# Optimization experiments

Hardware: AMD Instinct MI355X
Metric: run time of the kernel (lower is better)

## Reference

```python
import jax, jax.numpy as jnp
import numpy as np

CA, CZ, CS, CSI = 128, 128, 384, 256
NH, HD, NB, A = 8, 16, 6, 7
RMAX, SMAX = 32, 2
RELP_DIM = 4 * (RMAX + 1) + 1 + 2 * (SMAX + 1)  # 139


def make_relp(L):
    # single-chain relative-position features: [L, L, 139]
    i = jnp.arange(L)
    d = i[:, None] - i[None, :]
    a_rel_pos = jax.nn.one_hot(jnp.clip(d + RMAX, 0, 2 * RMAX), 2 * (RMAX + 1))
    d_tok = jnp.where(d == 0, RMAX, 2 * RMAX + 1)  # same-res only on diagonal
    a_rel_tok = jax.nn.one_hot(d_tok, 2 * (RMAX + 1))
    same_ent = jnp.ones((L, L, 1), jnp.float32)
    a_rel_chain = jax.nn.one_hot(jnp.full((L, L), SMAX), 2 * (SMAX + 1))
    return jnp.concatenate([a_rel_pos, a_rel_tok, same_ent, a_rel_chain], axis=-1)


def ln(x, g, b):
    m = x.mean(-1, keepdims=True)
    v = ((x - m) ** 2).mean(-1, keepdims=True)
    return (x - m) / jnp.sqrt(v + 1e-5) * g + b


def setup_inputs():
    key = jax.random.key(0)
    ks = iter(jax.random.split(key, 64))
    def p(*shape):
        return (jax.random.normal(next(ks), shape, jnp.float32) * 0.05)
    B, Ns, L = 1, 2, 384
    inp = dict(
        x_t=jax.random.normal(next(ks), (B, Ns, L, A, 3), jnp.float32),
        sigma=jax.random.uniform(next(ks), (B, Ns), jnp.float32),
        s_inputs=jax.random.normal(next(ks), (B, L, CSI), jnp.float32),
        s_trunk=jax.random.normal(next(ks), (B, L, CS), jnp.float32),
        z_trunk=jax.random.normal(next(ks), (B, L, L, CZ), jnp.float32),
        token_mask=jnp.ones((B, L), bool),
        s_in_w=p(CSI, CS), s_in_b=p(CS),
        relp_w=p(RELP_DIM, CZ), relp_b=p(CZ),
        t1_w=p(1, CS), t1_b=p(CS), t2_w=p(CS, CS), t2_b=p(CS),
        xp_w=p(3 * A, CA), xp_b=p(CA),
        s2a_w=p(CS, CA), s2a_b=p(CA),
        out_w=p(CA, 3 * A), out_b=p(3 * A),
        an_g=jnp.ones((NB, CA)), an_b=jnp.zeros((NB, CA)),
        zn_g=jnp.ones((NB, CZ)), zn_b=jnp.zeros((NB, CZ)),
        qw=p(NB, CA, CA), qb=p(NB, CA),
        kw=p(NB, CA, CA), kb=p(NB, CA),
        vw=p(NB, CA, CA), vb=p(NB, CA),
        zw=p(NB, CZ, NH), zb=p(NB, NH),
        ow=p(NB, CA, CA), ob=p(NB, CA),
        f1w=p(NB, CA, 4 * CA), f1b=p(NB, 4 * CA),
        f2w=p(NB, 4 * CA, CA), f2b=p(NB, CA),
    )
    return inp


def reference(x_t, sigma, s_inputs, s_trunk, z_trunk, token_mask,
              s_in_w, s_in_b, relp_w, relp_b, t1_w, t1_b, t2_w, t2_b,
              xp_w, xp_b, s2a_w, s2a_b, out_w, out_b,
              an_g, an_b, zn_g, zn_b, qw, qb, kw, kb, vw, vb,
              zw, zb, ow, ob, f1w, f1b, f2w, f2b):
    B, Ns, L = x_t.shape[:3]
    relp = make_relp(L)                                   # [L, L, 139]
    pair_z = z_trunk + relp @ relp_w + relp_b             # [B, L, L, CZ]
    s_cond = s_trunk + s_inputs @ s_in_w + s_in_b         # [B, L, CS]
    t_feat = jax.nn.silu(sigma.reshape(B * Ns, 1) @ t1_w + t1_b) @ t2_w + t2_b
    single_s = s_cond[:, None] + t_feat.reshape(B, Ns, CS)[:, :, None]  # [B,Ns,L,CS]
    a = x_t.reshape(B, Ns, L, 3 * A) @ xp_w + xp_b + single_s @ s2a_w + s2a_b
    a2 = a.reshape(B * Ns, L, CA)
    z2 = jnp.broadcast_to(pair_z[:, None], (B, Ns, L, L, CZ)).reshape(B * Ns, L, L, CZ)
    m = jnp.broadcast_to(token_mask[:, None], (B, Ns, L)).reshape(B * Ns, L)
    pair_mask = m[:, :, None] & m[:, None, :]             # [B*Ns, L, L]
    scale = 1.0 / np.sqrt(HD).astype(np.float32)
    for i in range(NB):
        an = ln(a2, an_g[i], an_b[i])
        zn = ln(z2, zn_g[i], zn_b[i])
        q = (an @ qw[i] + qb[i]).reshape(-1, L, NH, HD)
        k = (an @ kw[i] + kb[i]).reshape(-1, L, NH, HD)
        v = (an @ vw[i] + vb[i]).reshape(-1, L, NH, HD)
        logits = jnp.einsum('blhd,bmhd->bhlm', q, k) * scale
        bias = (zn @ zw[i] + zb[i]).transpose(0, 3, 1, 2)  # [B*Ns, NH, L, L]
        logits = jnp.where(pair_mask[:, None], logits + bias, -1e9)
        attn = jax.nn.softmax(logits, axis=-1)
        o = jnp.einsum('bhlm,bmhd->blhd', attn, v).reshape(-1, L, CA)
        a2 = a2 + (o @ ow[i] + ob[i])
        an2 = ln(a2, an_g[i], an_b[i])
        a2 = a2 + jax.nn.gelu(an2 @ f1w[i] + f1b[i], approximate=False) @ f2w[i] + f2b[i]
    vout = (a2 @ out_w + out_b).reshape(B, Ns, L, A, 3)
    return vout * token_mask[:, None, :, None, None].astype(vout.dtype)
```

## Files before the change

### kernel.cpp

```cpp
#include <hip/hip_runtime.h>
#include <math.h>

#define L 384
#define CA 128
#define NH 8
#define HD 16
#define NB 6
#define NS 2
#define NP (L*L)

typedef __attribute__((ext_vector_type(4))) float f32x4;
typedef __attribute__((ext_vector_type(8))) short s16x8;
typedef __attribute__((ext_vector_type(4))) unsigned short u16x4;
typedef unsigned short ushort_t;

__device__ inline unsigned short f2bf(float f){
  union { float f; unsigned int u; } v; v.f = f;
  unsigned int u = v.u;
  unsigned int r = u + 0x7FFF + ((u>>16)&1);
  return (unsigned short)(r>>16);
}
__device__ inline float bf2f(ushort_t u){
  union { float f; unsigned int i; } v; v.i = ((unsigned int)u)<<16; return v.f;
}

#define WT_LAYER 196608
__global__ __launch_bounds__(256) void k_prep(
    const float* qw, const float* kw, const float* vw,
    const float* f1w, const float* f2w, const float* ow,
    const float* relp_w, const float* relp_b,
    const float* s_in_w, const float* s2a_w,
    const float* sigma, const float* t1w, const float* t1b,
    const float* t2w, const float* t2b,
    const float* zng, const float* znb, const float* zw, const float* zb,
    ushort_t* wT, ushort_t* wzT, float* rbase, float* cb, float* t_feat,
    ushort_t* s_in_wT, ushort_t* s2a_wT){
  int b = blockIdx.x, t = threadIdx.x;
  if(b == 324){
    for(int idx=t; idx<6144; idx+=256){
      int h = idx>>7, c = idx&127;
      wzT[h*128+c] = f2bf(zng[(h>>3)*128+c]*zw[((h>>3)*128+c)*8+(h&7)]);
    }
    if(t<128) rbase[t] = relp_w[132*128+t] + relp_w[135*128+t] + relp_b[t];
    if(t<48){
      int blk=t>>3, hh=t&7;
      float acc = zb[t];
      for(int c=0;c<128;c++) acc += znb[blk*128+c]*zw[(blk*128+c)*8+hh];
      cb[t] = acc;
    }
    return;
  }
  if(b == 325){
    __shared__ float sil[2][384];
    for(int i=t;i<768;i+=256){
      int s=i/384, k=i%384;
      float x = sigma[s]*t1w[k] + t1b[k];
      sil[s][k] = x / (1.f + expf(-x));
    }
    __syncthreads();
    for(int o=t;o<768;o+=256){
      int s=o/384, c=o%384;
      float acc = t2b[c];
      for(int k=0;k<384;k++) acc += sil[s][k]*t2w[k*384+c];
      t_feat[s*384+c] = acc;
    }
    return;
  }
  __shared__ float tl[64][65];
  const float* src; ushort_t* dst;
  int M, N, k0, n0;
  if(b < 96){
    int mat = b>>2, li = mat>>2, wsel = mat&3, tile = b&3;
    const float* const ws_[4] = {qw, kw, vw, ow};
    const int off_[4] = {0, 16384, 32768, 180224};
    src = ws_[wsel] + (size_t)li*16384;
    dst = wT + (size_t)li*WT_LAYER + off_[wsel];
    M = 128; N = 128; k0 = (tile>>1)*64; n0 = (tile&1)*64;
  } else if(b < 192){
    int idx = b-96, li = idx>>4, tile = idx&15;
    src = f1w + (size_t)li*65536;
    dst = wT + (size_t)li*WT_LAYER + 49152;
    M = 128; N = 512; k0 = (tile>>3)*64; n0 = (tile&7)*64;
  } else if(b < 288){
    int idx = b-192, li = idx>>4, tile = idx&15;
    src = f2w + (size_t)li*65536;
    dst = wT + (size_t)li*WT_LAYER + 114688;
    M = 512; N = 128; k0 = (tile>>1)*64; n0 = (tile&1)*64;
  } else if(b < 312){
    int tile = b-288;
    src = s_in_w; dst = s_in_wT;
    M = 256; N = 384; k0 = (tile/6)*64; n0 = (tile%6)*64;
  } else {
    int tile = b-312;
    src = s2a_w; dst = s2a_wT;
    M = 384; N = 128; k0 = (tile>>1)*64; n0 = (tile&1)*64;
  }
  for(int i=t;i<4096;i+=256){
    int r=i>>6, c=i&63;
    tl[r][c] = src[(size_t)(k0+r)*N + n0+c];
  }
  __syncthreads();
  for(int i=t;i<4096;i+=256){
    int r=i>>6, c=i&63;
    dst[(size_t)(n0+r)*M + k0+c] = f2bf(tl[c][r]);
  }
}

__global__ __launch_bounds__(256) void k2_bias(
    const float* z_trunk, const float* relp_w, const float* rbase,
    const ushort_t* wzT, const float* cb, ushort_t* bias_all){
  __shared__ float lds_c[48][65];
  int t = threadIdx.x, lane = t&63, wv = t>>6;
  int rowf = lane&15, kg = lane>>4;
  int p = blockIdx.x*64 + wv*16 + rowf;
  int i = p/L, j = p - i*L, d = i - j;
  int r1 = d+32; r1 = r1<0?0:(r1>64?64:r1);
  int r2 = (d==0) ? 98 : 131;
  const float* zp  = z_trunk + (size_t)p*128;
  const float* w1p = relp_w + r1*128;
  const float* w2p = relp_w + r2*128;

  float val[4][8];
  float s = 0.f;
  #pragma unroll
  for(int ks=0; ks<4; ks++){
    int c0 = ks*32 + kg*8;
    f32x4 za = *(const f32x4*)(zp +c0), zb2 = *(const f32x4*)(zp +c0+4);
    f32x4 wa = *(const f32x4*)(w1p+c0), wb = *(const f32x4*)(w1p+c0+4);
    f32x4 ua = *(const f32x4*)(w2p+c0), ub = *(const f32x4*)(w2p+c0+4);
    f32x4 ra = *(const f32x4*)(rbase+c0), rb = *(const f32x4*)(rbase+c0+4);
    #pragma unroll
    for(int jj=0;jj<4;jj++){
      val[ks][jj]   = za[jj]+wa[jj]+ua[jj]+ra[jj];
      val[ks][jj+4] = zb2[jj]+wb[jj]+ub[jj]+rb[jj];
      s += val[ks][jj] + val[ks][jj+4];
    }
  }
  s += __shfl_xor(s,16,64); s += __shfl_xor(s,32,64);
  float mean = s*(1.f/128.f);
  float q2 = 0.f;
  #pragma unroll
  for(int ks=0; ks<4; ks++)
    #pragma unroll
    for(int jj=0;jj<8;jj++){ float dd = val[ks][jj]-mean; q2 += dd*dd; }
  q2 += __shfl_xor(q2,16,64); q2 += __shfl_xor(q2,32,64);
  float rstd = rsqrtf(q2*(1.f/128.f) + 1e-5f);

  s16x8 af[4];
  #pragma unroll
  for(int ks=0; ks<4; ks++)
    #pragma unroll
    for(int jj=0;jj<8;jj++) af[ks][jj] = (short)f2bf((val[ks][jj]-mean)*rstd);

  #pragma unroll
  for(int ht=0; ht<3; ht++){
    int col = ht*16 + rowf;
    float cbv = cb[col];
    f32x4 acc = {cbv,cbv,cbv,cbv};
    #pragma unroll
    for(int ks=0; ks<4; ks++){
      s16x8 bf = *(const s16x8*)&wzT[col*128 + ks*32 + kg*8];
      acc = __builtin_amdgcn_mfma_f32_16x16x32_bf16(af[ks], bf, acc, 0,0,0);
    }
    #pragma unroll
    for(int i2=0;i2<4;i2++) lds_c[col][wv*16 + kg*4 + i2] = acc[i2];
  }
  __syncthreads();
  int p0 = blockIdx.x*64;
  int i0 = p0/L, qt_ = i0>>4, q16 = i0&15, j0 = p0 - i0*L;
  for(int idx=t; idx<3072; idx+=256){
    int pl = idx>>6, c = idx&63;
    int li_ = pl>>3, h_ = pl&7;
    bias_all[(size_t)((li_*24+qt_)*8+h_)*6144 + q16*384 + j0 + c] = f2bf(lds_c[pl][c]);
  }
}

__device__ inline void qkv_project(ushort_t zh[16][152], const ushort_t* wTl,
                                   const float* qb, const float* kb, const float* vb,
                                   ushort_t* q_bf, ushort_t* k_bf, ushort_t* vT_bf,
                                   int s_idx, int lbase, int wv, int rowf, int kg){
  s16x8 af[4];
  #pragma unroll
  for(int ks=0;ks<4;ks++) af[ks] = *(const s16x8*)&zh[rowf][ks*32 + kg*8];
  #pragma unroll
  for(int u=0;u<6;u++){
    int unit = wv*6 + u;
    int proj = unit>>3, nt = unit&7;
    int col = nt*16 + rowf;
    const ushort_t* wp = wTl + proj*16384;
    const float* bias = proj==0? qb : (proj==1? kb : vb);
    float bv = bias[col];
    f32x4 acc = {bv,bv,bv,bv};
    #pragma unroll
    for(int ks=0;ks<4;ks++){
      s16x8 bf = *(const s16x8*)&wp[col*128 + ks*32 + kg*8];
      acc = __builtin_amdgcn_mfma_f32_16x16x32_bf16(af[ks], bf, acc, 0,0,0);
    }
    int sh = s_idx*NH + nt;
    if(proj==2){
      #pragma unroll
      for(int i2=0;i2<4;i2++)
        vT_bf[((size_t)sh*16 + rowf)*384 + lbase + kg*4 + i2] = f2bf(acc[i2]);
    } else {
      float sc = (proj==0)? 0.25f : 1.0f;
      ushort_t* outp = (proj==0)? q_bf : k_bf;
      #pragma unroll
      for(int i2=0;i2<4;i2++)
        outp[((size_t)sh*384 + lbase + kg*4 + i2)*16 + rowf] = f2bf(acc[i2]*sc);
    }
  }
}

__global__ __launch_bounds__(256) void k_qkv0(
    const float* x_t, const float* s_inputs, const float* s_trunk,
    const float* s_in_b, const ushort_t* s_in_wT,
    const float* s2a_b, const ushort_t* s2a_wT,
    const float* xp_w, const float* xp_b, const float* t_feat,
    const float* g, const float* bb,
    const ushort_t* wTl, const float* qb, const float* kb, const float* vb,
    float* a2, ushort_t* q_bf, ushort_t* k_bf, ushort_t* vT_bf){
  __shared__ ushort_t si[16][280];
  __shared__ ushort_t scb[16][408];
  __shared__ float xrow[16][21];
  __shared__ float a_new[16][132];
  __shared__ ushort_t zh[16][152];
  int t = threadIdx.x, lane = t&63, wv = t>>6;
  int rowf = lane&15, kg = lane>>4;
  int bid = blockIdx.x, s_idx = bid/24, lt = bid%24;
  int lr0 = lt*16;

  for(int i=t;i<16*256;i+=256){
    int r=i>>8, c=i&255;
    si[r][c] = f2bf(s_inputs[(size_t)(lr0+r)*256+c]);
  }
  for(int i=t;i<16*21;i+=256){
    int r=i/21, u=i%21;
    xrow[r][u] = x_t[((size_t)s_idx*L + lr0 + r)*21 + u];
  }
  __syncthreads();

  {
    s16x8 af1[8];
    #pragma unroll
    for(int ks=0;ks<8;ks++) af1[ks] = *(const s16x8*)&si[rowf][ks*32+kg*8];
    const float* tf = t_feat + s_idx*384;
    #pragma unroll
    for(int nn=0;nn<6;nn++){
      int col = (wv*6+nn)*16 + rowf;
      float bv = s_in_b[col];
      f32x4 acc = {bv,bv,bv,bv};
      #pragma unroll
      for(int ks=0;ks<8;ks++){
        s16x8 bf = *(const s16x8*)&s_in_wT[col*256 + ks*32 + kg*8];
        acc = __builtin_amdgcn_mfma_f32_16x16x32_bf16(af1[ks], bf, acc, 0,0,0);
      }
      float tfc = tf[col];
      #pragma unroll
      for(int i2=0;i2<4;i2++){
        int r = kg*4+i2;
        scb[r][col] = f2bf(acc[i2] + s_trunk[(size_t)(lr0+r)*384+col] + tfc);
      }
    }
  }
  __syncthreads();

  {
    s16x8 xf[12];
    #pragma unroll
    for(int ks=0;ks<12;ks++) xf[ks] = *(const s16x8*)&scb[rowf][ks*32+kg*8];
    #pragma unroll
    for(int nn=0;nn<2;nn++){
      int col = (wv*2+nn)*16 + rowf;
      float base = xp_b[col] + s2a_b[col];
      f32x4 acc;
      #pragma unroll
      for(int i2=0;i2<4;i2++){
        float xc = base;
        #pragma unroll
        for(int u=0;u<21;u++) xc += xrow[kg*4+i2][u]*xp_w[u*128+col];
        acc[i2] = xc;
      }
      #pragma unroll
      for(int ks=0;ks<12;ks++){
        s16x8 bf = *(const s16x8*)&s2a_wT[col*384 + ks*32 + kg*8];
        acc = __builtin_amdgcn_mfma_f32_16x16x32_bf16(xf[ks], bf, acc, 0,0,0);
      }
      #pragma unroll
      for(int i2=0;i2<4;i2++){
        int r = kg*4+i2;
        a_new[r][col] = acc[i2];
        a2[((size_t)(s_idx*L + lr0 + r))*128 + col] = acc[i2];
      }
    }
  }
  __syncthreads();

  {
    int row = t>>4, sub = t&15;
    const float* xp = &a_new[row][sub*8];
    f32x4 x0 = *(const f32x4*)xp;
    f32x4 x1 = *(const f32x4*)(xp+4);
    float s = x0[0]+x0[1]+x0[2]+x0[3]+x1[0]+x1[1]+x1[2]+x1[3];
    s += __shfl_xor(s,1,64); s += __shfl_xor(s,2,64);
    s += __shfl_xor(s,4,64); s += __shfl_xor(s,8,64);
    float mean = s*(1.f/128.f);
    float q2 = 0.f;
    #pragma unroll
    for(int jj=0;jj<4;jj++){ float d0=x0[jj]-mean, d1=x1[jj]-mean; q2 += d0*d0+d1*d1; }
    q2 += __shfl_xor(q2,1,64); q2 += __shfl_xor(q2,2,64);
    q2 += __shfl_xor(q2,4,64); q2 += __shfl_xor(q2,8,64);
    float rstd = rsqrtf(q2*(1.f/128.f)+1e-5f);
    int c0 = sub*8;
    f32x4 g0 = *(const f32x4*)(g+c0), g1 = *(const f32x4*)(g+c0+4);
    f32x4 b0 = *(const f32x4*)(bb+c0), b1 = *(const f32x4*)(bb+c0+4);
    s16x8 pack;
    #pragma unroll
    for(int jj=0;jj<4;jj++){
      pack[jj]   = (short)f2bf((x0[jj]-mean)*rstd*g0[jj]+b0[jj]);
      pack[jj+4] = (short)f2bf((x1[jj]-mean)*rstd*g1[jj]+b1[jj]);
    }
    *(s16x8*)&zh[row][c0] = pack;
  }
  __syncthreads();
  qkv_project(zh, wTl, qb, kb, vb, q_bf, k_bf, vT_bf, s_idx, lr0, wv, rowf, kg);
}

__global__ __launch_bounds__(1024) void k_fused(
    float* a2, const float* an_g, const float* an_b, const ushort_t* wT,
    const float* qb_all, const float* kb_all, const float* vb_all,
    const float* ob_all, const float* f1b_all, const float* f2b_all,
    ushort_t* q_bf, ushort_t* k_bf, ushort_t* vT_bf,
    const ushort_t* bias_all, const float* out_w, const float* out_b,
    float* out, int li){
  __shared__ float orow[16][132];
  __shared__ float ocomb[8][16][20];
  __shared__ float lcomb[8][16];
  union SM {
    struct {
      ushort_t bias[8][16][392];
      ushort_t P[16][16][72];
    } fl;
    struct {
      float a_new[16][132];
      ushort_t zh[16][152];
      ushort_t h_lds[16][536];
      float fcomb[8][16][20];
    } post;
  };
  __shared__ SM sm;

  int t = threadIdx.x, lane = t&63, wv = t>>6;
  int rowf = lane&15, kg = lane>>4;
  int bid = blockIdx.x, s_idx = bid/24, qt = bid%24;
  int r0 = bid*16;
  const ushort_t* wTl = wT + (size_t)li*WT_LAYER;
  const float* g  = an_g + li*128;
  const float* bb = an_b + li*128;

  {
    const ushort_t* btile = bias_all + (size_t)(li*24+qt)*8*6144;
    #pragma unroll
    for(int it=0; it<6; it++){
      int idx = t + it*1024;
      int row2 = idx/48, seg = idx%48;
      *(s16x8*)&sm.fl.bias[row2>>4][row2&15][seg*8] =
          *(const s16x8*)&btile[(size_t)row2*384 + seg*8];
    }
  }
  __syncthreads();

  {
    int h = wv>>1, kh = wv&1;
    int sh = s_idx*NH + h;
    ushort_t (*Pw)[72] = sm.fl.P[wv];
    s16x8 qf = {0,0,0,0,0,0,0,0};
    if(kg < 2) qf = *(const s16x8*)&q_bf[((size_t)sh*384 + qt*16 + rowf)*16 + kg*8];
    const ushort_t* kp = k_bf + (size_t)sh*384*16;
    const ushort_t* vp = vT_bf + ((size_t)sh*16 + rowf)*384;

    f32x4 o0 = {0,0,0,0}, o1 = {0,0,0,0};
    float l_acc = 0.f;
    for(int c=0;c<3;c++){
      int key0 = kh*192 + c*64;
      f32x4 st[4];
      #pragma unroll
      for(int t4=0;t4<4;t4++){
        s16x8 kf = {0,0,0,0,0,0,0,0};
        if(kg < 2) kf = *(const s16x8*)&kp[((size_t)(key0 + t4*16 + rowf))*16 + kg*8];
        u16x4 bb4 = *(const u16x4*)&sm.fl.bias[h][rowf][key0 + t4*16 + kg*4];
        f32x4 cin;
        #pragma unroll
        for(int jj=0;jj<4;jj++) cin[jj] = bf2f(bb4[jj]);
        st[t4] = __builtin_amdgcn_mfma_f32_16x16x32_bf16(kf, qf, cin, 0,0,0);
      }
      #pragma unroll
      for(int t4=0;t4<4;t4++){
        float p0 = __expf(st[t4][0]), p1 = __expf(st[t4][1]);
        float p2 = __expf(st[t4][2]), p3 = __expf(st[t4][3]);
        l_acc += (p0+p1)+(p2+p3);
        u16x4 pk = {f2bf(p0), f2bf(p1), f2bf(p2), f2bf(p3)};
        *(u16x4*)&Pw[rowf][t4*16 + kg*4] = pk;
      }
      {
        s16x8 pa = *(const s16x8*)&Pw[rowf][kg*8];
        s16x8 vbf = *(const s16x8*)&vp[key0 + kg*8];
        o0 = __builtin_amdgcn_mfma_f32_16x16x32_bf16(pa, vbf, o0, 0,0,0);
        s16x8 pb = *(const s16x8*)&Pw[rowf][32 + kg*8];
        s16x8 vbf2 = *(const s16x8*)&vp[key0 + 32 + kg*8];
        o1 = __builtin_amdgcn_mfma_f32_16x16x32_bf16(pb, vbf2, o1, 0,0,0);
      }
    }
    f32x4 o_acc = o0 + o1;
    l_acc += __shfl_xor(l_acc, 16, 64);
    l_acc += __shfl_xor(l_acc, 32, 64);
    if(kh==1){
      #pragma unroll
      for(int i2=0;i2<4;i2++) ocomb[h][kg*4+i2][rowf] = o_acc[i2];
      if(kg==0) lcomb[h][rowf] = l_acc;
    }
    __syncthreads();
    if(kh==0){
      l_acc += lcomb[h][rowf];
      #pragma unroll
      for(int i2=0;i2<4;i2++) o_acc[i2] += ocomb[h][kg*4+i2][rowf];
      float inv = 1.f / l_acc;
      #pragma unroll
      for(int i2=0;i2<4;i2++){
        float invq = __shfl(inv, kg*4 + i2, 64);
        orow[kg*4+i2][h*16 + rowf] = o_acc[i2]*invq;
      }
    }
  }
  __syncthreads();

  if(wv < 8){
    s16x8 af[4];
    #pragma unroll
    for(int ks=0;ks<4;ks++){
      f32x4 v0 = *(const f32x4*)&orow[rowf][ks*32+kg*8];
      f32x4 v1 = *(const f32x4*)&orow[rowf][ks*32+kg*8+4];
      s16x8 p;
      #pragma unroll
      for(int jj=0;jj<4;jj++){ p[jj] = (short)f2bf(v0[jj]); p[jj+4] = (short)f2bf(v1[jj]); }
      af[ks] = p;
    }
    const ushort_t* wo = wTl + 180224;
    const float* obp = ob_all + li*128;
    int col = wv*16 + rowf;
    float bv = obp[col];
    f32x4 acc = {bv,bv,bv,bv};
    f32x4 accB = {0,0,0,0};
    #pragma unroll
    for(int ks=0;ks<2;ks++){
      s16x8 bf = *(const s16x8*)&wo[col*128 + ks*32 + kg*8];
      acc = __builtin_amdgcn_mfma_f32_16x16x32_bf16(af[ks], bf, acc, 0,0,0);
      s16x8 bf2 = *(const s16x8*)&wo[col*128 + (ks+2)*32 + kg*8];
      accB = __builtin_amdgcn_mfma_f32_16x16x32_bf16(af[ks+2], bf2, accB, 0,0,0);
    }
    acc += accB;
    #pragma unroll
    for(int i2=0;i2<4;i2++){
      int r = kg*4+i2;
      sm.post.a_new[r][col] = a2[(size_t)(r0+r)*128 + col] + acc[i2];
    }
  }
  __syncthreads();

  {
    int row = wv, c0 = lane*2;
    float x0 = sm.post.a_new[row][c0], x1 = sm.post.a_new[row][c0+1];
    float s = x0+x1;
    s += __shfl_xor(s,1,64); s += __shfl_xor(s,2,64); s += __shfl_xor(s,4,64);
    s += __shfl_xor(s,8,64); s += __shfl_xor(s,16,64); s += __shfl_xor(s,32,64);
    float mean = s*(1.f/128.f);
    float d0=x0-mean, d1=x1-mean;
    float q2 = d0*d0+d1*d1;
    q2 += __shfl_xor(q2,1,64); q2 += __shfl_xor(q2,2,64); q2 += __shfl_xor(q2,4,64);
    q2 += __shfl_xor(q2,8,64); q2 += __shfl_xor(q2,16,64); q2 += __shfl_xor(q2,32,64);
    float rstd = rsqrtf(q2*(1.f/128.f)+1e-5f);
    unsigned int pk = (unsigned int)f2bf(d0*rstd*g[c0]+bb[c0])
                    | ((unsigned int)f2bf(d1*rstd*g[c0+1]+bb[c0+1])<<16);
    *(unsigned int*)&sm.post.zh[row][c0] = pk;
  }
  __syncthreads();

  {
    s16x8 xf[4];
    #pragma unroll
    for(int ks=0;ks<4;ks++) xf[ks] = *(const s16x8*)&sm.post.zh[rowf][ks*32 + kg*8];
    const ushort_t* w1 = wTl + 49152;
    const float* f1bp = f1b_all + li*512;
    #pragma unroll
    for(int nn=0; nn<2; nn++){
      int col = (wv*2+nn)*16 + rowf;
      float bv = f1bp[col];
      f32x4 acc = {bv,bv,bv,bv};
      #pragma unroll
      for(int ks=0;ks<4;ks++){
        s16x8 bf = *(const s16x8*)&w1[col*128 + ks*32 + kg*8];
        acc = __builtin_amdgcn_mfma_f32_16x16x32_bf16(xf[ks], bf, acc, 0,0,0);
      }
      #pragma unroll
      for(int i2=0;i2<4;i2++){
        float x = acc[i2];
        float ge = 0.5f*x*(1.f + erff(x*0.70710678f));
        sm.post.h_lds[kg*4+i2][col] = f2bf(ge);
      }
    }
  }
  __syncthreads();

  {
    const ushort_t* w2 = wTl + 114688;
    const float* f2bp = f2b_all + li*128;
    int ct = wv>>1, kh2 = wv&1;
    int col2 = ct*16 + rowf;
    float bv = kh2? 0.f : f2bp[col2];
    f32x4 accA = {bv,bv,bv,bv};
    f32x4 accB = {0,0,0,0};
    int ks0 = kh2*8;
    #pragma unroll
    for(int kk=0; kk<4; kk++){
      s16x8 hfA = *(const s16x8*)&sm.post.h_lds[rowf][(ks0+kk)*32 + kg*8];
      s16x8 bfA = *(const s16x8*)&w2[col2*512 + (ks0+kk)*32 + kg*8];
      accA = __builtin_amdgcn_mfma_f32_16x16x32_bf16(hfA, bfA, accA, 0,0,0);
      s16x8 hfB = *(const s16x8*)&sm.post.h_lds[rowf][(ks0+kk+4)*32 + kg*8];
      s16x8 bfB = *(const s16x8*)&w2[col2*512 + (ks0+kk+4)*32 + kg*8];
      accB = __builtin_amdgcn_mfma_f32_16x16x32_bf16(hfB, bfB, accB, 0,0,0);
    }
    accA += accB;
    if(kh2==1){
      #pragma unroll
      for(int i2=0;i2<4;i2++) sm.post.fcomb[ct][kg*4+i2][rowf] = accA[i2];
    }
    __syncthreads();
    if(kh2==0){
      #pragma unroll
      for(int i2=0;i2<4;i2++){
        int r = kg*4+i2;
        float fin = sm.post.a_new[r][col2] + accA[i2] + sm.post.fcomb[ct][r][rowf];
        a2[(size_t)(r0+r)*128 + col2] = fin;
        sm.post.a_new[r][col2] = fin;
      }
    }
  }
  __syncthreads();

  if(li < NB-1){
    const float* g2  = an_g + (li+1)*128;
    const float* bb2 = an_b + (li+1)*128;
    {
      int row = wv, c0 = lane*2;
      float x0 = sm.post.a_new[row][c0], x1 = sm.post.a_new[row][c0+1];
      float s = x0+x1;
      s += __shfl_xor(s,1,64); s += __shfl_xor(s,2,64); s += __shfl_xor(s,4,64);
      s += __shfl_xor(s,8,64); s += __shfl_xor(s,16,64); s += __shfl_xor(s,32,64);
      float mean = s*(1.f/128.f);
      float d0=x0-mean, d1=x1-mean;
      float q2 = d0*d0+d1*d1;
      q2 += __shfl_xor(q2,1,64); q2 += __shfl_xor(q2,2,64); q2 += __shfl_xor(q2,4,64);
      q2 += __shfl_xor(q2,8,64); q2 += __shfl_xor(q2,16,64); q2 += __shfl_xor(q2,32,64);
      float rstd = rsqrtf(q2*(1.f/128.f)+1e-5f);
      unsigned int pk = (unsigned int)f2bf(d0*rstd*g2[c0]+bb2[c0])
                      | ((unsigned int)f2bf(d1*rstd*g2[c0+1]+bb2[c0+1])<<16);
      *(unsigned int*)&sm.post.zh[row][c0] = pk;
    }
    __syncthreads();
    {
      const ushort_t* wTn = wT + (size_t)(li+1)*WT_LAYER;
      const float* qb2 = qb_all + (li+1)*128;
      const float* kb2 = kb_all + (li+1)*128;
      const float* vb2 = vb_all + (li+1)*128;
      s16x8 af[4];
      #pragma unroll
      for(int ks=0;ks<4;ks++) af[ks] = *(const s16x8*)&sm.post.zh[rowf][ks*32 + kg*8];
      #pragma unroll
      for(int u=0;u<2;u++){
        int unit = wv + u*16;
        if(unit < 24){
          int proj = unit>>3, nt = unit&7;
          int col = nt*16 + rowf;
          const ushort_t* wp = wTn + proj*16384;
          const float* bias = proj==0? qb2 : (proj==1? kb2 : vb2);
          float bv = bias[col];
          f32x4 acc = {bv,bv,bv,bv};
          #pragma unroll
          for(int ks=0;ks<4;ks++){
            s16x8 bf = *(const s16x8*)&wp[col*128 + ks*32 + kg*8];
            acc = __builtin_amdgcn_mfma_f32_16x16x32_bf16(af[ks], bf, acc, 0,0,0);
          }
          int sh = s_idx*NH + nt;
          if(proj==2){
            #pragma unroll
            for(int i2=0;i2<4;i2++)
              vT_bf[((size_t)sh*16 + rowf)*384 + qt*16 + kg*4 + i2] = f2bf(acc[i2]);
          } else {
            float sc = (proj==0)? 0.25f : 1.0f;
            ushort_t* outp = (proj==0)? q_bf : k_bf;
            #pragma unroll
            for(int i2=0;i2<4;i2++)
              outp[((size_t)sh*384 + qt*16 + kg*4 + i2)*16 + rowf] = f2bf(acc[i2]*sc);
          }
        }
      }
    }
  } else {
    for(int idx=t; idx<336; idx+=1024){
      int r = idx/21, c = idx%21;
      float acc = out_b[c];
      #pragma unroll 8
      for(int kk=0;kk<128;kk++) acc += sm.post.a_new[r][kk]*out_w[kk*21+c];
      out[(size_t)(r0+r)*21 + c] = acc;
    }
  }
}

extern "C" void kernel_launch(void* const* d_in, const int* in_sizes, int n_in,
                              void* d_out, int out_size, void* d_ws, size_t ws_size,
                              hipStream_t stream){
  const float* x_t      = (const float*)d_in[0];
  const float* sigma    = (const float*)d_in[1];
  const float* s_inputs = (const float*)d_in[2];
  const float* s_trunk  = (const float*)d_in[3];
  const float* z_trunk  = (const float*)d_in[4];
  const float* s_in_w = (const float*)d_in[6];
  const float* s_in_b = (const float*)d_in[7];
  const float* relp_w = (const float*)d_in[8];
  const float* relp_b = (const float*)d_in[9];
  const float* t1_w = (const float*)d_in[10];
  const float* t1_b = (const float*)d_in[11];
  const float* t2_w = (const float*)d_in[12];
  const float* t2_b = (const float*)d_in[13];
  const float* xp_w = (const float*)d_in[14];
  const float* xp_b = (const float*)d_in[15];
  const float* s2a_w = (const float*)d_in[16];
  const float* s2a_b = (const float*)d_in[17];
  const float* out_w = (const float*)d_in[18];
  const float* out_b = (const float*)d_in[19];
  const float* an_g = (const float*)d_in[20];
  const float* an_b = (const float*)d_in[21];
  const float* zn_g = (const float*)d_in[22];
  const float* zn_b = (const float*)d_in[23];
  const float* qw = (const float*)d_in[24];
  const float* qb = (const float*)d_in[25];
  const float* kw = (const float*)d_in[26];
  const float* kb = (const float*)d_in[27];
  const float* vw = (const float*)d_in[28];
  const float* vb = (const float*)d_in[29];
  const float* zw = (const float*)d_in[30];
  const float* zb = (const float*)d_in[31];
  const float* ow = (const float*)d_in[32];
  const float* ob = (const float*)d_in[33];
  const float* f1w = (const float*)d_in[34];
  const float* f1b = (const float*)d_in[35];
  const float* f2w = (const float*)d_in[36];
  const float* f2b = (const float*)d_in[37];

  float* ws = (float*)d_ws;
  ushort_t* bias_all = (ushort_t*)ws;
  float* cb     = ws + (size_t)24*NP;
  float* t_feat = cb + 48;
  float* a2     = t_feat + 768;
  float* rbase  = a2 + (size_t)NS*L*CA;
  ushort_t* wT      = (ushort_t*)(rbase + 128);
  ushort_t* wzT     = wT + (size_t)6*WT_LAYER;
  ushort_t* q_bf    = wzT + 6144;
  ushort_t* k_bf    = q_bf + 98304;
  ushort_t* vT_bf   = k_bf + 98304;
  ushort_t* s_in_wT = vT_bf + 98304;
  ushort_t* s2a_wT  = s_in_wT + 98304;
  float* outp = (float*)d_out;

  k_prep<<<326,256,0,stream>>>(qw,kw,vw,f1w,f2w,ow,relp_w,relp_b,s_in_w,s2a_w,
                               sigma,t1_w,t1_b,t2_w,t2_b,zn_g,zn_b,zw,zb,
                               wT,wzT,rbase,cb,t_feat,s_in_wT,s2a_wT);
  k2_bias<<<NP/64,256,0,stream>>>(z_trunk,relp_w,rbase,wzT,cb,bias_all);

  k_qkv0<<<48,256,0,stream>>>(x_t,s_inputs,s_trunk,s_in_b,s_in_wT,
                              s2a_b,s2a_wT,xp_w,xp_b,t_feat,
                              an_g, an_b, wT, qb, kb, vb,
                              a2, q_bf, k_bf, vT_bf);
  for(int i=0;i<NB;i++){
    k_fused<<<48,1024,0,stream>>>(a2, an_g, an_b, wT,
        qb, kb, vb, ob, f1b, f2b,
        q_bf, k_bf, vT_bf, bias_all,
        out_w, out_b, outp, i);
  }
}
```

Measured before the change: 233.9 us.

## Stage per-layer weights into swizzled LDS before MFMA in post-attention path

Before each post-attention GEMM (out-proj, FFN1 halves, FFN2 halves, next-layer QKV), the weight tiles are cooperatively copied from global into a new 96KB shared buffer with an XOR swizzle. MFMA operands are then read from LDS instead of directly from global memory. The FFN work is split into phases to fit the staging buffer, which adds barriers and raises LDS usage. The prep transpose kernel is also restructured to batch its loads into registers.

```diff
diff --git a/kernel.cpp b/kernel.cpp
--- a/kernel.cpp
+++ b/kernel.cpp
@@ -22,6 +22,10 @@
 }
 __device__ inline float bf2f(ushort_t u){
   union { float f; unsigned int i; } v; v.i = ((unsigned int)u)<<16; return v.f;
+}
+
+__device__ inline s16x8 ldw(const ushort_t* base, int col, int K, int k){
+  return *(const s16x8*)&base[col*K + (k ^ ((col&7)<<3))];
 }
 
 #define WT_LAYER 196608
@@ -95,14 +99,28 @@
     src = s2a_w; dst = s2a_wT;
     M = 384; N = 128; k0 = (tile>>1)*64; n0 = (tile&1)*64;
   }
-  for(int i=t;i<4096;i+=256){
-    int r=i>>6, c=i&63;
-    tl[r][c] = src[(size_t)(k0+r)*N + n0+c];
-  }
-  __syncthreads();
-  for(int i=t;i<4096;i+=256){
-    int r=i>>6, c=i&63;
-    dst[(size_t)(n0+r)*M + k0+c] = f2bf(tl[c][r]);
+  float v[16];
+  #pragma unroll
+  for(int it=0;it<16;it++){
+    int i = t + it*256;
+    v[it] = src[(size_t)(k0+(i>>6))*N + n0+(i&63)];
+  }
+  #pragma unroll
+  for(int it=0;it<16;it++){
+    int i = t + it*256;
+    tl[i>>6][i&63] = v[it];
+  }
+  __syncthreads();
+  ushort_t o16[16];
+  #pragma unroll
+  for(int it=0;it<16;it++){
+    int i = t + it*256;
+    o16[it] = f2bf(tl[i&63][i>>6]);
+  }
+  #pragma unroll
+  for(int it=0;it<16;it++){
+    int i = t + it*256;
+    dst[(size_t)(n0+(i>>6))*M + k0+(i&63)] = o16[it];
   }
 }
 
@@ -345,6 +363,7 @@
       ushort_t zh[16][152];
       ushort_t h_lds[16][536];
       float fcomb[8][16][20];
+      ushort_t wst[49152];
     } post;
   };
   __shared__ SM sm;
@@ -433,6 +452,26 @@
   }
   __syncthreads();
 
+  {
+    const ushort_t* wo = wTl + 180224;
+    #pragma unroll
+    for(int it=0; it<2; it++){
+      int idx = t + it*1024;
+      int col = idx>>4, seg = idx&15;
+      s16x8 v = *(const s16x8*)&wo[col*128 + seg*8];
+      *(s16x8*)&sm.post.wst[col*128 + ((seg*8) ^ ((col&7)<<3))] = v;
+    }
+    const ushort_t* w1 = wTl + 49152;
+    #pragma unroll
+    for(int it=0; it<4; it++){
+      int idx = t + it*1024;
+      int col = idx>>4, seg = idx&15;
+      s16x8 v = *(const s16x8*)&w1[col*128 + seg*8];
+      *(s16x8*)&sm.post.wst[16384 + col*128 + ((seg*8) ^ ((col&7)<<3))] = v;
+    }
+  }
+  __syncthreads();
+
   if(wv < 8){
     s16x8 af[4];
     #pragma unroll
@@ -444,7 +483,6 @@
       for(int jj=0;jj<4;jj++){ p[jj] = (short)f2bf(v0[jj]); p[jj+4] = (short)f2bf(v1[jj]); }
       af[ks] = p;
     }
-    const ushort_t* wo = wTl + 180224;
     const float* obp = ob_all + li*128;
     int col = wv*16 + rowf;
     float bv = obp[col];
@@ -452,10 +490,10 @@
     f32x4 accB = {0,0,0,0};
     #pragma unroll
     for(int ks=0;ks<2;ks++){
-      s16x8 bf = *(const s16x8*)&wo[col*128 + ks*32 + kg*8];
-      acc = __builtin_amdgcn_mfma_f32_16x16x32_bf16(af[ks], bf, acc, 0,0,0);
-      s16x8 bf2 = *(const s16x8*)&wo[col*128 + (ks+2)*32 + kg*8];
-      accB = __builtin_amdgcn_mfma_f32_16x16x32_bf16(af[ks+2], bf2, accB, 0,0,0);
+      acc  = __builtin_amdgcn_mfma_f32_16x16x32_bf16(af[ks],
+                ldw(sm.post.wst, col, 128, ks*32+kg*8), acc, 0,0,0);
+      accB = __builtin_amdgcn_mfma_f32_16x16x32_bf16(af[ks+2],
+                ldw(sm.post.wst, col, 128, (ks+2)*32+kg*8), accB, 0,0,0);
     }
     acc += accB;
     #pragma unroll
@@ -484,64 +522,164 @@
   }
   __syncthreads();
 
-  {
-    s16x8 xf[4];
-    #pragma unroll
-    for(int ks=0;ks<4;ks++) xf[ks] = *(const s16x8*)&sm.post.zh[rowf][ks*32 + kg*8];
+  s16x8 xf[4];
+  #pragma unroll
+  for(int ks=0;ks<4;ks++) xf[ks] = *(const s16x8*)&sm.post.zh[rowf][ks*32 + kg*8];
+  const float* f1bp = f1b_all + li*512;
+
+  {
+    int coll = wv*16 + rowf;
+    float bv = f1bp[coll];
+    f32x4 acc = {bv,bv,bv,bv};
+    #pragma unroll
+    for(int ks=0;ks<4;ks++)
+      acc = __builtin_amdgcn_mfma_f32_16x16x32_bf16(xf[ks],
+              ldw(sm.post.wst+16384, coll, 128, ks*32+kg*8), acc, 0,0,0);
+    #pragma unroll
+    for(int i2=0;i2<4;i2++){
+      float x = acc[i2];
+      float ge = 0.5f*x*(1.f + erff(x*0.70710678f));
+      sm.post.h_lds[kg*4+i2][coll] = f2bf(ge);
+    }
+  }
+  __syncthreads();
+
+  {
     const ushort_t* w1 = wTl + 49152;
-    const float* f1bp = f1b_all + li*512;
-    #pragma unroll
-    for(int nn=0; nn<2; nn++){
-      int col = (wv*2+nn)*16 + rowf;
-      float bv = f1bp[col];
-      f32x4 acc = {bv,bv,bv,bv};
-      #pragma unroll
-      for(int ks=0;ks<4;ks++){
-        s16x8 bf = *(const s16x8*)&w1[col*128 + ks*32 + kg*8];
-        acc = __builtin_amdgcn_mfma_f32_16x16x32_bf16(xf[ks], bf, acc, 0,0,0);
-      }
-      #pragma unroll
-      for(int i2=0;i2<4;i2++){
-        float x = acc[i2];
-        float ge = 0.5f*x*(1.f + erff(x*0.70710678f));
-        sm.post.h_lds[kg*4+i2][col] = f2bf(ge);
-      }
-    }
-  }
-  __syncthreads();
-
-  {
-    const ushort_t* w2 = wTl + 114688;
-    const float* f2bp = f2b_all + li*128;
-    int ct = wv>>1, kh2 = wv&1;
+    #pragma unroll
+    for(int it=0; it<4; it++){
+      int idx = t + it*1024;
+      int col = idx>>4, seg = idx&15;
+      s16x8 v = *(const s16x8*)&w1[(256+col)*128 + seg*8];
+      *(s16x8*)&sm.post.wst[col*128 + ((seg*8) ^ ((col&7)<<3))] = v;
+    }
+  }
+  __syncthreads();
+
+  {
+    int coll = wv*16 + rowf;
+    int colg = 256 + coll;
+    float bv = f1bp[colg];
+    f32x4 acc = {bv,bv,bv,bv};
+    #pragma unroll
+    for(int ks=0;ks<4;ks++)
+      acc = __builtin_amdgcn_mfma_f32_16x16x32_bf16(xf[ks],
+              ldw(sm.post.wst, coll, 128, ks*32+kg*8), acc, 0,0,0);
+    #pragma unroll
+    for(int i2=0;i2<4;i2++){
+      float x = acc[i2];
+      float ge = 0.5f*x*(1.f + erff(x*0.70710678f));
+      sm.post.h_lds[kg*4+i2][colg] = f2bf(ge);
+    }
+  }
+  __syncthreads();
+
+  const ushort_t* w2 = wTl + 114688;
+  const float* f2bp = f2b_all + li*128;
+  {
+    #pragma unroll
+    for(int it=0; it<4; it++){
+      int idx = t + it*1024;
+      int col = idx>>6, seg = idx&63;
+      s16x8 v = *(const s16x8*)&w2[col*512 + seg*8];
+      *(s16x8*)&sm.post.wst[col*512 + ((seg*8) ^ ((col&7)<<3))] = v;
+    }
+  }
+  __syncthreads();
+
+  int ct = wv>>1, kh2 = wv&1;
+  if(ct < 4){
     int col2 = ct*16 + rowf;
     float bv = kh2? 0.f : f2bp[col2];
-    f32x4 accA = {bv,bv,bv,bv};
-    f32x4 accB = {0,0,0,0};
+    f32x4 accA = {bv,bv,bv,bv}, accB = {0,0,0,0};
     int ks0 = kh2*8;
     #pragma unroll
     for(int kk=0; kk<4; kk++){
       s16x8 hfA = *(const s16x8*)&sm.post.h_lds[rowf][(ks0+kk)*32 + kg*8];
-      s16x8 bfA = *(const s16x8*)&w2[col2*512 + (ks0+kk)*32 + kg*8];
-      accA = __builtin_amdgcn_mfma_f32_16x16x32_bf16(hfA, bfA, accA, 0,0,0);
+      accA = __builtin_amdgcn_mfma_f32_16x16x32_bf16(hfA,
+               ldw(sm.post.wst, col2, 512, (ks0+kk)*32+kg*8), accA, 0,0,0);
       s16x8 hfB = *(const s16x8*)&sm.post.h_lds[rowf][(ks0+kk+4)*32 + kg*8];
-      s16x8 bfB = *(const s16x8*)&w2[col2*512 + (ks0+kk+4)*32 + kg*8];
-      accB = __builtin_amdgcn_mfma_f32_16x16x32_bf16(hfB, bfB, accB, 0,0,0);
+      accB = __builtin_amdgcn_mfma_f32_16x16x32_bf16(hfB,
+               ldw(sm.post.wst, col2, 512, (ks0+kk+4)*32+kg*8), accB, 0,0,0);
     }
     accA += accB;
     if(kh2==1){
       #pragma unroll
       for(int i2=0;i2<4;i2++) sm.post.fcomb[ct][kg*4+i2][rowf] = accA[i2];
-    }
-    __syncthreads();
-    if(kh2==0){
+    } else {
+      #pragma unroll
+      for(int i2=0;i2<4;i2++) sm.post.fcomb[ct+4][kg*4+i2][rowf] = accA[i2];
+    }
+  }
+  __syncthreads();
+
+  {
+    #pragma unroll
+    for(int it=0; it<4; it++){
+      int idx = t + it*1024;
+      int col = idx>>6, seg = idx&63;
+      s16x8 v = *(const s16x8*)&w2[(64+col)*512 + seg*8];
+      *(s16x8*)&sm.post.wst[col*512 + ((seg*8) ^ ((col&7)<<3))] = v;
+    }
+    if(ct < 4 && kh2 == 0){
+      int col2 = ct*16 + rowf;
       #pragma unroll
       for(int i2=0;i2<4;i2++){
         int r = kg*4+i2;
-        float fin = sm.post.a_new[r][col2] + accA[i2] + sm.post.fcomb[ct][r][rowf];
+        float fin = sm.post.a_new[r][col2] + sm.post.fcomb[ct+4][r][rowf]
+                  + sm.post.fcomb[ct][r][rowf];
         a2[(size_t)(r0+r)*128 + col2] = fin;
         sm.post.a_new[r][col2] = fin;
       }
+    }
+  }
+  __syncthreads();
+
+  if(ct >= 4){
+    int col2 = ct*16 + rowf;
+    int coll = col2 - 64;
+    float bv = kh2? 0.f : f2bp[col2];
+    f32x4 accA = {bv,bv,bv,bv}, accB = {0,0,0,0};
+    int ks0 = kh2*8;
+    #pragma unroll
+    for(int kk=0; kk<4; kk++){
+      s16x8 hfA = *(const s16x8*)&sm.post.h_lds[rowf][(ks0+kk)*32 + kg*8];
+      accA = __builtin_amdgcn_mfma_f32_16x16x32_bf16(hfA,
+               ldw(sm.post.wst, coll, 512, (ks0+kk)*32+kg*8), accA, 0,0,0);
+      s16x8 hfB = *(const s16x8*)&sm.post.h_lds[rowf][(ks0+kk+4)*32 + kg*8];
+      accB = __builtin_amdgcn_mfma_f32_16x16x32_bf16(hfB,
+               ldw(sm.post.wst, coll, 512, (ks0+kk+4)*32+kg*8), accB, 0,0,0);
+    }
+    accA += accB;
+    if(kh2==1){
+      #pragma unroll
+      for(int i2=0;i2<4;i2++) sm.post.fcomb[ct-4][kg*4+i2][rowf] = accA[i2];
+    } else {
+      #pragma unroll
+      for(int i2=0;i2<4;i2++) sm.post.fcomb[ct][kg*4+i2][rowf] = accA[i2];
+    }
+  }
+  __syncthreads();
+
+  if(ct >= 4 && kh2 == 0){
+    int col2 = ct*16 + rowf;
+    #pragma unroll
+    for(int i2=0;i2<4;i2++){
+      int r = kg*4+i2;
+      float fin = sm.post.a_new[r][col2] + sm.post.fcomb[ct][r][rowf]
+                + sm.post.fcomb[ct-4][r][rowf];
+      a2[(size_t)(r0+r)*128 + col2] = fin;
+      sm.post.a_new[r][col2] = fin;
+    }
+  }
+  if(li < NB-1){
+    const ushort_t* wTn = wT + (size_t)(li+1)*WT_LAYER;
+    #pragma unroll
+    for(int it=0; it<6; it++){
+      int idx = t + it*1024;
+      int col = idx>>4, seg = idx&15;
+      s16x8 v = *(const s16x8*)&wTn[col*128 + seg*8];
+      *(s16x8*)&sm.post.wst[col*128 + ((seg*8) ^ ((col&7)<<3))] = v;
     }
   }
   __syncthreads();
@@ -567,7 +705,6 @@
     }
     __syncthreads();
     {
-      const ushort_t* wTn = wT + (size_t)(li+1)*WT_LAYER;
       const float* qb2 = qb_all + (li+1)*128;
       const float* kb2 = kb_all + (li+1)*128;
       const float* vb2 = vb_all + (li+1)*128;
@@ -580,15 +717,13 @@
         if(unit < 24){
           int proj = unit>>3, nt = unit&7;
           int col = nt*16 + rowf;
-          const ushort_t* wp = wTn + proj*16384;
           const float* bias = proj==0? qb2 : (proj==1? kb2 : vb2);
           float bv = bias[col];
           f32x4 acc = {bv,bv,bv,bv};
           #pragma unroll
-          for(int ks=0;ks<4;ks++){
-            s16x8 bf = *(const s16x8*)&wp[col*128 + ks*32 + kg*8];
-            acc = __builtin_amdgcn_mfma_f32_16x16x32_bf16(af[ks], bf, acc, 0,0,0);
-          }
+          for(int ks=0;ks<4;ks++)
+            acc = __builtin_amdgcn_mfma_f32_16x16x32_bf16(af[ks],
+                    ldw(sm.post.wst + proj*16384, col, 128, ks*32+kg*8), acc, 0,0,0);
           int sh = s_idx*NH + nt;
           if(proj==2){
             #pragma unroll
```

Result: slower. 242.1 us (+3.5%).

## Restructure prep: tiny dependency kernel, merge weight transposes into bias kernel

Applied to the files above, without the earlier changes.

Only the small wzT/rbase/cb computation that the pair-bias kernel depends on now runs in a single-block kernel. The weight transposes and the timestep MLP are merged into the large pair-bias launch as extra blocks. The serial timestep MLP, previously one block with a 384-long dot per thread, is spread over 12 blocks with split-K reduction. The cb reduction is split four ways, and the transpose loads are batched into registers. The aim is to remove the long tail of the serial prep blocks and overlap the transposes with the bias work, at the cost of a larger, more branchy mega-kernel.

```diff
diff --git a/kernel.cpp b/kernel.cpp
--- a/kernel.cpp
+++ b/kernel.cpp
@@ -25,153 +25,174 @@
 }
 
 #define WT_LAYER 196608
-__global__ __launch_bounds__(256) void k_prep(
+
+__global__ __launch_bounds__(256) void k_pre0(
+    const float* zng, const float* znb, const float* zw, const float* zb,
+    const float* relp_w, const float* relp_b,
+    ushort_t* wzT, float* rbase, float* cb){
+  int t = threadIdx.x;
+  __shared__ float part[48][5];
+  for(int idx=t; idx<6144; idx+=256){
+    int h = idx>>7, c = idx&127;
+    wzT[h*128+c] = f2bf(zng[(h>>3)*128+c]*zw[((h>>3)*128+c)*8+(h&7)]);
+  }
+  if(t<128) rbase[t] = relp_w[132*128+t] + relp_w[135*128+t] + relp_b[t];
+  if(t<192){
+    int h = t>>2, ch = t&3, blk = h>>3, hh = h&7;
+    float acc = 0.f;
+    #pragma unroll 8
+    for(int c=ch*32; c<ch*32+32; c++)
+      acc += znb[blk*128+c]*zw[(blk*128+c)*8+hh];
+    part[h][ch] = acc;
+  }
+  __syncthreads();
+  if(t<48) cb[t] = zb[t] + part[t][0]+part[t][1]+part[t][2]+part[t][3];
+}
+
+__global__ __launch_bounds__(256) void k_mega(
+    const float* z_trunk, const float* relp_w, const float* rbase,
+    const ushort_t* wzT, const float* cb, ushort_t* bias_all,
     const float* qw, const float* kw, const float* vw,
     const float* f1w, const float* f2w, const float* ow,
-    const float* relp_w, const float* relp_b,
     const float* s_in_w, const float* s2a_w,
+    ushort_t* wT, ushort_t* s_in_wT, ushort_t* s2a_wT,
     const float* sigma, const float* t1w, const float* t1b,
-    const float* t2w, const float* t2b,
-    const float* zng, const float* znb, const float* zw, const float* zb,
-    ushort_t* wT, ushort_t* wzT, float* rbase, float* cb, float* t_feat,
-    ushort_t* s_in_wT, ushort_t* s2a_wT){
-  int b = blockIdx.x, t = threadIdx.x;
-  if(b == 324){
-    for(int idx=t; idx<6144; idx+=256){
-      int h = idx>>7, c = idx&127;
-      wzT[h*128+c] = f2bf(zng[(h>>3)*128+c]*zw[((h>>3)*128+c)*8+(h&7)]);
-    }
-    if(t<128) rbase[t] = relp_w[132*128+t] + relp_w[135*128+t] + relp_b[t];
-    if(t<48){
-      int blk=t>>3, hh=t&7;
-      float acc = zb[t];
-      for(int c=0;c<128;c++) acc += znb[blk*128+c]*zw[(blk*128+c)*8+hh];
-      cb[t] = acc;
-    }
-    return;
-  }
-  if(b == 325){
-    __shared__ float sil[2][384];
-    for(int i=t;i<768;i+=256){
-      int s=i/384, k=i%384;
-      float x = sigma[s]*t1w[k] + t1b[k];
-      sil[s][k] = x / (1.f + expf(-x));
+    const float* t2w, const float* t2b, float* t_feat){
+  __shared__ float smem[4160];
+  int bid = blockIdx.x, t = threadIdx.x;
+
+  if(bid < 2304){
+    float (*lds_c)[65] = (float(*)[65])smem;
+    int lane = t&63, wv = t>>6;
+    int rowf = lane&15, kg = lane>>4;
+    int p = bid*64 + wv*16 + rowf;
+    int i = p/L, j = p - i*L, d = i - j;
+    int r1 = d+32; r1 = r1<0?0:(r1>64?64:r1);
+    int r2 = (d==0) ? 98 : 131;
+    const float* zp  = z_trunk + (size_t)p*128;
+    const float* w1p = relp_w + r1*128;
+    const float* w2p = relp_w + r2*128;
+
+    float val[4][8];
+    float s = 0.f;
+    #pragma unroll
+    for(int ks=0; ks<4; ks++){
+      int c0 = ks*32 + kg*8;
+      f32x4 za = *(const f32x4*)(zp +c0), zb2 = *(const f32x4*)(zp +c0+4);
+      f32x4 wa = *(const f32x4*)(w1p+c0), wb = *(const f32x4*)(w1p+c0+4);
+      f32x4 ua = *(const f32x4*)(w2p+c0), ub = *(const f32x4*)(w2p+c0+4);
+      f32x4 ra = *(const f32x4*)(rbase+c0), rb = *(const f32x4*)(rbase+c0+4);
+      #pragma unroll
+      for(int jj=0;jj<4;jj++){
+        val[ks][jj]   = za[jj]+wa[jj]+ua[jj]+ra[jj];
+        val[ks][jj+4] = zb2[jj]+wb[jj]+ub[jj]+rb[jj];
+        s += val[ks][jj] + val[ks][jj+4];
+      }
+    }
+    s += __shfl_xor(s,16,64); s += __shfl_xor(s,32,64);
+    float mean = s*(1.f/128.f);
+    float q2 = 0.f;
+    #pragma unroll
+    for(int ks=0; ks<4; ks++)
+      #pragma unroll
+      for(int jj=0;jj<8;jj++){ float dd = val[ks][jj]-mean; q2 += dd*dd; }
+    q2 += __shfl_xor(q2,16,64); q2 += __shfl_xor(q2,32,64);
+    float rstd = rsqrtf(q2*(1.f/128.f) + 1e-5f);
+
+    s16x8 af[4];
+    #pragma unroll
+    for(int ks=0; ks<4; ks++)
+      #pragma unroll
+      for(int jj=0;jj<8;jj++) af[ks][jj] = (short)f2bf((val[ks][jj]-mean)*rstd);
+
+    #pragma unroll
+    for(int ht=0; ht<3; ht++){
+      int col = ht*16 + rowf;
+      float cbv = cb[col];
+      f32x4 acc = {cbv,cbv,cbv,cbv};
+      #pragma unroll
+      for(int ks=0; ks<4; ks++){
+        s16x8 bf = *(const s16x8*)&wzT[col*128 + ks*32 + kg*8];
+        acc = __builtin_amdgcn_mfma_f32_16x16x32_bf16(af[ks], bf, acc, 0,0,0);
+      }
+      #pragma unroll
+      for(int i2=0;i2<4;i2++) lds_c[col][wv*16 + kg*4 + i2] = acc[i2];
     }
     __syncthreads();
-    for(int o=t;o<768;o+=256){
-      int s=o/384, c=o%384;
-      float acc = t2b[c];
-      for(int k=0;k<384;k++) acc += sil[s][k]*t2w[k*384+c];
-      t_feat[s*384+c] = acc;
-    }
-    return;
-  }
-  __shared__ float tl[64][65];
-  const float* src; ushort_t* dst;
-  int M, N, k0, n0;
-  if(b < 96){
-    int mat = b>>2, li = mat>>2, wsel = mat&3, tile = b&3;
-    const float* const ws_[4] = {qw, kw, vw, ow};
-    const int off_[4] = {0, 16384, 32768, 180224};
-    src = ws_[wsel] + (size_t)li*16384;
-    dst = wT + (size_t)li*WT_LAYER + off_[wsel];
-    M = 128; N = 128; k0 = (tile>>1)*64; n0 = (tile&1)*64;
-  } else if(b < 192){
-    int idx = b-96, li = idx>>4, tile = idx&15;
-    src = f1w + (size_t)li*65536;
-    dst = wT + (size_t)li*WT_LAYER + 49152;
-    M = 128; N = 512; k0 = (tile>>3)*64; n0 = (tile&7)*64;
-  } else if(b < 288){
-    int idx = b-192, li = idx>>4, tile = idx&15;
-    src = f2w + (size_t)li*65536;
-    dst = wT + (size_t)li*WT_LAYER + 114688;
-    M = 512; N = 128; k0 = (tile>>1)*64; n0 = (tile&1)*64;
-  } else if(b < 312){
-    int tile = b-288;
-    src = s_in_w; dst = s_in_wT;
-    M = 256; N = 384; k0 = (tile/6)*64; n0 = (tile%6)*64;
+    int p0 = bid*64;
+    int i0 = p0/L, qt_ = i0>>4, q16 = i0&15, j0 = p0 - i0*L;
+    for(int idx=t; idx<3072; idx+=256){
+      int pl = idx>>6, c = idx&63;
+      int li_ = pl>>3, h_ = pl&7;
+      bias_all[(size_t)((li_*24+qt_)*8+h_)*6144 + q16*384 + j0 + c] = f2bf(lds_c[pl][c]);
+    }
+  } else if(bid < 2628){
+    float (*tl)[65] = (float(*)[65])smem;
+    int b = bid - 2304;
+    const float* src; ushort_t* dst;
+    int M, N, k0, n0;
+    if(b < 96){
+      int mat = b>>2, li = mat>>2, wsel = mat&3, tile = b&3;
+      const float* const ws_[4] = {qw, kw, vw, ow};
+      const int off_[4] = {0, 16384, 32768, 180224};
+      src = ws_[wsel] + (size_t)li*16384;
+      dst = wT + (size_t)li*WT_LAYER + off_[wsel];
+      M = 128; N = 128; k0 = (tile>>1)*64; n0 = (tile&1)*64;
+    } else if(b < 192){
+      int idx = b-96, li = idx>>4, tile = idx&15;
+      src = f1w + (size_t)li*65536;
+      dst = wT + (size_t)li*WT_LAYER + 49152;
+      M = 128; N = 512; k0 = (tile>>3)*64; n0 = (tile&7)*64;
+    } else if(b < 288){
+      int idx = b-192, li = idx>>4, tile = idx&15;
+      src = f2w + (size_t)li*65536;
+      dst = wT + (size_t)li*WT_LAYER + 114688;
+      M = 512; N = 128; k0 = (tile>>1)*64; n0 = (tile&1)*64;
+    } else if(b < 312){
+      int tile = b-288;
+      src = s_in_w; dst = s_in_wT;
+      M = 256; N = 384; k0 = (tile/6)*64; n0 = (tile%6)*64;
+    } else {
+      int tile = b-312;
+      src = s2a_w; dst = s2a_wT;
+      M = 384; N = 128; k0 = (tile>>1)*64; n0 = (tile&1)*64;
+    }
+    float v[16];
+    #pragma unroll
+    for(int it=0;it<16;it++){
+      int i = t + it*256;
+      v[it] = src[(size_t)(k0+(i>>6))*N + n0+(i&63)];
+    }
+    #pragma unroll
+    for(int it=0;it<16;it++){
+      int i = t + it*256;
+      tl[i>>6][i&63] = v[it];
+    }
+    __syncthreads();
+    #pragma unroll
+    for(int it=0;it<16;it++){
+      int i = t + it*256;
+      dst[(size_t)(n0+(i>>6))*M + k0+(i&63)] = f2bf(tl[i&63][i>>6]);
+    }
   } else {
-    int tile = b-312;
-    src = s2a_w; dst = s2a_wT;
-    M = 384; N = 128; k0 = (tile>>1)*64; n0 = (tile&1)*64;
-  }
-  for(int i=t;i<4096;i+=256){
-    int r=i>>6, c=i&63;
-    tl[r][c] = src[(size_t)(k0+r)*N + n0+c];
-  }
-  __syncthreads();
-  for(int i=t;i<4096;i+=256){
-    int r=i>>6, c=i&63;
-    dst[(size_t)(n0+r)*M + k0+c] = f2bf(tl[c][r]);
-  }
-}
-
-__global__ __launch_bounds__(256) void k2_bias(
-    const float* z_trunk, const float* relp_w, const float* rbase,
-    const ushort_t* wzT, const float* cb, ushort_t* bias_all){
-  __shared__ float lds_c[48][65];
-  int t = threadIdx.x, lane = t&63, wv = t>>6;
-  int rowf = lane&15, kg = lane>>4;
-  int p = blockIdx.x*64 + wv*16 + rowf;
-  int i = p/L, j = p - i*L, d = i - j;
-  int r1 = d+32; r1 = r1<0?0:(r1>64?64:r1);
-  int r2 = (d==0) ? 98 : 131;
-  const float* zp  = z_trunk + (size_t)p*128;
-  const float* w1p = relp_w + r1*128;
-  const float* w2p = relp_w + r2*128;
-
-  float val[4][8];
-  float s = 0.f;
-  #pragma unroll
-  for(int ks=0; ks<4; ks++){
-    int c0 = ks*32 + kg*8;
-    f32x4 za = *(const f32x4*)(zp +c0), zb2 = *(const f32x4*)(zp +c0+4);
-    f32x4 wa = *(const f32x4*)(w1p+c0), wb = *(const f32x4*)(w1p+c0+4);
-    f32x4 ua = *(const f32x4*)(w2p+c0), ub = *(const f32x4*)(w2p+c0+4);
-    f32x4 ra = *(const f32x4*)(rbase+c0), rb = *(const f32x4*)(rbase+c0+4);
-    #pragma unroll
-    for(int jj=0;jj<4;jj++){
-      val[ks][jj]   = za[jj]+wa[jj]+ua[jj]+ra[jj];
-      val[ks][jj+4] = zb2[jj]+wb[jj]+ub[jj]+rb[jj];
-      s += val[ks][jj] + val[ks][jj+4];
-    }
-  }
-  s += __shfl_xor(s,16,64); s += __shfl_xor(s,32,64);
-  float mean = s*(1.f/128.f);
-  float q2 = 0.f;
-  #pragma unroll
-  for(int ks=0; ks<4; ks++)
-    #pragma unroll
-    for(int jj=0;jj<8;jj++){ float dd = val[ks][jj]-mean; q2 += dd*dd; }
-  q2 += __shfl_xor(q2,16,64); q2 += __shfl_xor(q2,32,64);
-  float rstd = rsqrtf(q2*(1.f/128.f) + 1e-5f);
-
-  s16x8 af[4];
-  #pragma unroll
-  for(int ks=0; ks<4; ks++)
-    #pragma unroll
-    for(int jj=0;jj<8;jj++) af[ks][jj] = (short)f2bf((val[ks][jj]-mean)*rstd);
-
-  #pragma unroll
-  for(int ht=0; ht<3; ht++){
-    int col = ht*16 + rowf;
-    float cbv = cb[col];
-    f32x4 acc = {cbv,cbv,cbv,cbv};
-    #pragma unroll
-    for(int ks=0; ks<4; ks++){
-      s16x8 bf = *(const s16x8*)&wzT[col*128 + ks*32 + kg*8];
-      acc = __builtin_amdgcn_mfma_f32_16x16x32_bf16(af[ks], bf, acc, 0,0,0);
-    }
-    #pragma unroll
-    for(int i2=0;i2<4;i2++) lds_c[col][wv*16 + kg*4 + i2] = acc[i2];
-  }
-  __syncthreads();
-  int p0 = blockIdx.x*64;
-  int i0 = p0/L, qt_ = i0>>4, q16 = i0&15, j0 = p0 - i0*L;
-  for(int idx=t; idx<3072; idx+=256){
-    int pl = idx>>6, c = idx&63;
-    int li_ = pl>>3, h_ = pl&7;
-    bias_all[(size_t)((li_*24+qt_)*8+h_)*6144 + q16*384 + j0 + c] = f2bf(lds_c[pl][c]);
+    int j = bid - 2628;
+    int s = j/6, c0 = (j%6)*64;
+    float sg = sigma[s];
+    for(int i=t; i<384; i+=256){
+      float x = sg*t1w[i] + t1b[i];
+      smem[i] = x / (1.f + expf(-x));
+    }
+    __syncthreads();
+    int col = c0 + (t&63), ch = t>>6;
+    float acc = 0.f;
+    #pragma unroll 8
+    for(int k=ch*96; k<ch*96+96; k++)
+      acc += smem[k]*t2w[(size_t)k*384+col];
+    smem[384 + ch*64 + (t&63)] = acc;
+    __syncthreads();
+    if(t<64)
+      t_feat[s*384 + c0 + t] = t2b[c0+t]
+        + smem[384+t] + smem[448+t] + smem[512+t] + smem[576+t];
   }
 }
 
@@ -671,11 +692,11 @@
   ushort_t* s2a_wT  = s_in_wT + 98304;
   float* outp = (float*)d_out;
 
-  k_prep<<<326,256,0,stream>>>(qw,kw,vw,f1w,f2w,ow,relp_w,relp_b,s_in_w,s2a_w,
-                               sigma,t1_w,t1_b,t2_w,t2_b,zn_g,zn_b,zw,zb,
-                               wT,wzT,rbase,cb,t_feat,s_in_wT,s2a_wT);
-  k2_bias<<<NP/64,256,0,stream>>>(z_trunk,relp_w,rbase,wzT,cb,bias_all);
-
+  k_pre0<<<1,256,0,stream>>>(zn_g,zn_b,zw,zb,relp_w,relp_b,wzT,rbase,cb);
+  k_mega<<<2640,256,0,stream>>>(z_trunk,relp_w,rbase,wzT,cb,bias_all,
+                                qw,kw,vw,f1w,f2w,ow,s_in_w,s2a_w,
+                                wT,s_in_wT,s2a_wT,
+                                sigma,t1_w,t1_b,t2_w,t2_b,t_feat);
   k_qkv0<<<48,256,0,stream>>>(x_t,s_inputs,s_trunk,s_in_b,s_in_wT,
                               s2a_b,s2a_wT,xp_w,xp_b,t_feat,
                               an_g, an_b, wT, qb, kb, vb,
```

After: 210.8 us. -9.9%, faster.
